# Optimization experiments

Hardware: AMD Instinct MI355X
Metric: run time of the kernel (lower is better)

Reference implementation:

```python
import jax, jax.numpy as jnp
import numpy as np

D, H, T, K = 512, 8, 4, 64   # dim, n_heads, n_tasks, topk_n
HD = D // H
PRUNE, EPS = 1e-3, 1e-8


def _ln(x, g, b, eps=1e-5):
    m = jnp.mean(x, axis=-1, keepdims=True)
    v = jnp.mean((x - m) ** 2, axis=-1, keepdims=True)
    return (x - m) * jax.lax.rsqrt(v + eps) * g + b


def setup_inputs() -> dict:
    key = jax.random.key(0)
    ks = jax.random.split(key, 5)
    B, N = 16, 8192
    tokens = jax.random.normal(ks[0], (B, N, D), jnp.float32)
    key_padding_mask = jax.random.uniform(ks[1], (B, N)) < 0.1  # True marks padding
    q = jax.random.normal(ks[2], (1, T, D), jnp.float32) * 0.02
    in_proj_w = jax.random.normal(ks[3], (3 * D, D), jnp.float32) / np.sqrt(D).astype(np.float32)
    in_proj_b = jnp.zeros((3 * D,), jnp.float32)
    pre_g = jnp.ones((D,), jnp.float32)
    pre_b = jnp.zeros((D,), jnp.float32)
    q_g = jnp.ones((D,), jnp.float32)
    q_b = jnp.zeros((D,), jnp.float32)
    log_tau = jnp.asarray(np.log(0.3), jnp.float32)
    return dict(tokens=tokens, key_padding_mask=key_padding_mask, q=q,
                in_proj_w=in_proj_w, in_proj_b=in_proj_b,
                pre_g=pre_g, pre_b=pre_b, q_g=q_g, q_b=q_b, log_tau=log_tau)


def reference(tokens, key_padding_mask, q, in_proj_w, in_proj_b,
              pre_g, pre_b, q_g, q_b, log_tau):
    B, N, _ = tokens.shape
    kpm = key_padding_mask  # [B,N], True = pad

    normed = _ln(tokens, pre_g, pre_b)                       # [B,N,D]
    tau = jnp.clip(jnp.exp(log_tau), 0.1, 10.0)
    query = _ln(q, q_g, q_b) / tau                           # [1,T,D]

    wq, wk, wv = in_proj_w[:D], in_proj_w[D:2 * D], in_proj_w[2 * D:]
    bq, bk, bv = in_proj_b[:D], in_proj_b[D:2 * D], in_proj_b[2 * D:]

    qp = (query[0] @ wq.T + bq).reshape(T, H, HD)            # [T,H,hd]
    kp = (normed @ wk.T + bk).reshape(B, N, H, HD)           # [B,N,H,hd]

    scores = jnp.einsum('thd,bnhd->bhtn', qp, kp) / np.float32(np.sqrt(HD))
    scores = jnp.where(kpm[:, None, None, :], -jnp.inf, scores)
    attn = jax.nn.softmax(scores, axis=-1)                   # [B,H,T,N]

    alpha = attn.mean(axis=1)                                # [B,T,N]
    alpha = jnp.where(kpm[:, None, :], 0.0, alpha)
    alpha = alpha / jnp.maximum(alpha.sum(-1, keepdims=True), EPS)

    # prune below threshold, with argmax one-hot fallback if everything pruned
    a = jnp.where(alpha < PRUNE, 0.0, alpha)
    a = jnp.where(kpm[:, None, :], 0.0, a)
    s = a.sum(-1, keepdims=True)
    need_fallback = s <= EPS                                 # [B,T,1]
    base = jnp.where(kpm[:, None, :], -1.0, alpha)
    onehot = jax.nn.one_hot(jnp.argmax(base, axis=-1), N, dtype=a.dtype)  # [B,T,N]
    a = jnp.where(need_fallback, onehot, a)
    a = jnp.where(kpm[:, None, :], 0.0, a)
    alpha = a / jnp.maximum(a.sum(-1, keepdims=True), EPS)

    # pool source: tie_mha_v projection of normed inputs
    pool_source = normed @ wv.T + bv                         # [B,N,D]

    # top-k gather + renorm weighting
    topv, topi = jax.lax.top_k(alpha, K)                     # [B,T,K]
    selected = jnp.take_along_axis(pool_source[:, None, :, :], topi[..., None], axis=2)  # [B,T,K,D]
    w = topv / jnp.maximum(topv.sum(-1, keepdims=True), EPS)
    pooled = (w[..., None] * selected).sum(axis=2)           # [B,T,D]
    return pooled
```

## Files before the change

kernel.cpp:

```cpp
#include <hip/hip_runtime.h>
#include <math.h>

#define Dd   512
#define Hh   8
#define Tt   4
#define HDd  64
#define Bb   16
#define Nn   8192
#define HTc  32
#define KS   64
#define NTOK (Bb*Nn)
#define PRUNEc 0.001f
#define EPSc   1e-8f

#define WS_C1     0u
#define WS_C0     128u
#define WS_M      2048u
#define WS_L      4096u
#define WS_TOPW   6144u
#define WS_TOPI   22528u
#define WS_FLAG   38912u
#define WS_G2H    65536u
#define WS_G2M    98304u
#define WS_G2L    131072u
#define WS_MEAN   163840u
#define WS_INV    688128u
#define WS_MASK8  1212416u
#define WS_SCORES 2097152u

typedef __attribute__((ext_vector_type(8)))  short short8v;
typedef __attribute__((ext_vector_type(16))) float f32x16;

__device__ __forceinline__ void split3(float x, unsigned &h, unsigned &m, unsigned &l){
  unsigned u  = __float_as_uint(x);
  unsigned uh = u & 0xFFFF0000u;
  float rh = x - __uint_as_float(uh);
  unsigned um = __float_as_uint(rh) & 0xFFFF0000u;
  float rm = rh - __uint_as_float(um);
  unsigned ul = __float_as_uint(rm) & 0xFFFF0000u;
  h = uh; m = um; l = ul;
}

__device__ __forceinline__ void split3x8(float4 v0, float4 v1,
                                         short8v &h, short8v &m, short8v &l){
  union { short8v s; unsigned u[4]; } H, M, L;
  float a[8] = {v0.x,v0.y,v0.z,v0.w,v1.x,v1.y,v1.z,v1.w};
  #pragma unroll
  for (int w = 0; w < 4; ++w){
    unsigned ha, ma, la, hb, mb, lb;
    split3(a[2*w],   ha, ma, la);
    split3(a[2*w+1], hb, mb, lb);
    H.u[w] = (ha>>16) | (hb & 0xFFFF0000u);
    M.u[w] = (ma>>16) | (mb & 0xFFFF0000u);
    L.u[w] = (la>>16) | (lb & 0xFFFF0000u);
  }
  h = H.s; m = M.s; l = L.s;
}

__device__ __forceinline__ int chkw(unsigned v){
  return (v == 0x3f800000u) ? 2 : ((v & ~1u) ? 1 : 0);
}
__global__ void tap_detect(const uint4* mraw, int* flag){
  int tid = threadIdx.x;
  if (tid == 0) *flag = 0;
  __syncthreads();
  int f = 0;
  #pragma unroll
  for (int i = 0; i < 8; ++i){
    uint4 v = mraw[tid + i*1024];
    f |= chkw(v.x) | chkw(v.y) | chkw(v.z) | chkw(v.w);
  }
  if (f) atomicOr(flag, f);
}

__global__ void tap_mask(const void* mraw, const int* flag, unsigned char* m8){
  int i = blockIdx.x*256 + threadIdx.x;
  int fl = *flag;
  unsigned char m;
  if (fl & 2)      m = (((const float*)mraw)[i] != 0.0f);
  else if (fl & 1) m = (((const unsigned char*)mraw)[i] != 0);
  else             m = (((const int*)mraw)[i] != 0);
  m8[i] = m;
}

__global__ void tap_prep(const float* q, const float* ipw, const float* ipb,
                         const float* pre_g, const float* pre_b,
                         const float* q_g, const float* q_b, const float* log_tau,
                         unsigned short* G2h, unsigned short* G2m, unsigned short* G2l,
                         float* C1, float* C0){
  __shared__ float query[Tt][Dd];
  __shared__ float qps[HDd];
  __shared__ float red[256];
  int tid = threadIdx.x;
  int ht = blockIdx.x;
  int h = ht >> 2, t = ht & 3;
  float tau = expf(log_tau[0]);
  tau = fminf(fmaxf(tau, 0.1f), 10.0f);
  float itau = 1.0f / tau;
  int wv = tid >> 6, lane = tid & 63;
  {
    const float* qr = q + wv*Dd;
    float s = 0.f, ss = 0.f;
    for (int j = lane; j < Dd; j += 64){ float x = qr[j]; s += x; ss += x*x; }
    #pragma unroll
    for (int off = 32; off; off >>= 1){ s += __shfl_down(s, off); ss += __shfl_down(ss, off); }
    s = __shfl(s, 0); ss = __shfl(ss, 0);
    float mean = s * (1.f/Dd);
    float var  = ss * (1.f/Dd) - mean*mean;
    float inv  = rsqrtf(var + 1e-5f);
    for (int j = lane; j < Dd; j += 64){
      float x = qr[j];
      query[wv][j] = ((x - mean)*inv*q_g[j] + q_b[j]) * itau;
    }
  }
  __syncthreads();
  {
    int d = tid >> 2, sub = tid & 3;
    int i = h*HDd + d;
    const float* wrow = ipw + (size_t)i*Dd;
    float acc = 0.f;
    int j0 = sub*128;
    for (int j = 0; j < 128; ++j) acc += query[t][j0+j]*wrow[j0+j];
    red[tid] = acc;
    __syncthreads();
    if (sub == 0) qps[d] = red[tid]+red[tid+1]+red[tid+2]+red[tid+3] + ipb[i];
    __syncthreads();
  }
  float c1p = 0.f, c0p = 0.f;
  for (int jj = 0; jj < 2; ++jj){
    int j = tid + jj*256;
    float acc = 0.f;
    #pragma unroll 8
    for (int d = 0; d < HDd; ++d)
      acc += qps[d] * ipw[(size_t)(Dd + h*HDd + d)*Dd + j];
    float w2 = acc * 0.125f;
    float g2 = w2 * pre_g[j];
    unsigned uh, um, ul;
    split3(g2, uh, um, ul);
    G2h[ht*Dd + j] = (unsigned short)(uh >> 16);
    G2m[ht*Dd + j] = (unsigned short)(um >> 16);
    G2l[ht*Dd + j] = (unsigned short)(ul >> 16);
    float geff = __uint_as_float(uh) + __uint_as_float(um) + __uint_as_float(ul);
    c1p += geff;
    c0p += w2 * pre_b[j];
  }
  if (tid < HDd) c0p += qps[tid] * ipb[Dd + h*HDd + tid] * 0.125f;
  red[tid] = c1p; __syncthreads();
  for (int s = 128; s; s >>= 1){ if (tid < s) red[tid] += red[tid+s]; __syncthreads(); }
  if (tid == 0) C1[ht] = red[0];
  __syncthreads();
  red[tid] = c0p; __syncthreads();
  for (int s = 128; s; s >>= 1){ if (tid < s) red[tid] += red[tid+s]; __syncthreads(); }
  if (tid == 0) C0[ht] = red[0];
}

__global__ __launch_bounds__(256, 4) void tap_scores(
    const float* __restrict__ tokens,
    const unsigned short* __restrict__ G2h, const unsigned short* __restrict__ G2m,
    const unsigned short* __restrict__ G2l,
    const float* __restrict__ C1, const float* __restrict__ C0,
    float* __restrict__ scores, float* __restrict__ meanw, float* __restrict__ invw){
  int tid   = threadIdx.x;
  int lane  = tid & 63, wv = tid >> 6;
  int col   = lane & 31;
  int bhalf = lane >> 5;
  size_t t0 = (size_t)blockIdx.x * 128;
  int brow  = (wv << 5) | col;
  const float* __restrict__ xrow = tokens + (t0 + brow)*(size_t)Dd;
  int abase = (col << 9) | (bhalf << 3);

  f32x16 acc;
  #pragma unroll
  for (int i = 0; i < 16; ++i) acc[i] = 0.f;
  float ps = 0.f, pss = 0.f;

  for (int c = 0; c < 8; ++c){
    #pragma unroll
    for (int kc = 0; kc < 4; ++kc){
      int k0 = (c << 6) | (kc << 4) | (bhalf << 3);
      float4 v0 = *(const float4*)(xrow + k0);
      float4 v1 = *(const float4*)(xrow + k0 + 4);
      int ga = abase + (c << 6) + (kc << 4);
      short8v ah = *(const short8v*)(G2h + ga);
      short8v am = *(const short8v*)(G2m + ga);
      short8v al = *(const short8v*)(G2l + ga);
      ps  += v0.x+v0.y+v0.z+v0.w + v1.x+v1.y+v1.z+v1.w;
      pss += v0.x*v0.x+v0.y*v0.y+v0.z*v0.z+v0.w*v0.w
           + v1.x*v1.x+v1.y*v1.y+v1.z*v1.z+v1.w*v1.w;
      short8v bh, bm, bl;
      split3x8(v0, v1, bh, bm, bl);
      acc = __builtin_amdgcn_mfma_f32_32x32x16_bf16(ah, bh, acc, 0, 0, 0);
      acc = __builtin_amdgcn_mfma_f32_32x32x16_bf16(am, bh, acc, 0, 0, 0);
      acc = __builtin_amdgcn_mfma_f32_32x32x16_bf16(ah, bm, acc, 0, 0, 0);
      acc = __builtin_amdgcn_mfma_f32_32x32x16_bf16(am, bm, acc, 0, 0, 0);
      acc = __builtin_amdgcn_mfma_f32_32x32x16_bf16(al, bh, acc, 0, 0, 0);
      acc = __builtin_amdgcn_mfma_f32_32x32x16_bf16(ah, bl, acc, 0, 0, 0);
    }
  }
  ps  += __shfl_xor(ps, 32);
  pss += __shfl_xor(pss, 32);
  float mean = ps * (1.f/512.f);
  float var  = pss * (1.f/512.f) - mean*mean;
  float inv  = rsqrtf(var + 1e-5f);
  if (bhalf == 0){ meanw[t0 + brow] = mean; invw[t0 + brow] = inv; }
  int b = (int)(t0 >> 13);
  int n = (int)(t0 & 8191) + brow;
  #pragma unroll
  for (int r = 0; r < 16; ++r){
    int ht = (r & 3) + ((r >> 2) << 3) + (bhalf << 2);
    float sc = inv*(acc[r] - mean*C1[ht]) + C0[ht];
    scores[(((size_t)(b*HTc + ht)) << 13) + n] = sc;
  }
}

__global__ void tap_norm(const float* __restrict__ scores, const unsigned char* __restrict__ m8,
                         float* __restrict__ mrow, float* __restrict__ lrow){
  int R = blockIdx.x;
  int b = R >> 5;
  const float* srow = scores + (size_t)R*Nn;
  const unsigned char* mk = m8 + b*Nn;
  int tid = threadIdx.x;
  int wv = tid >> 6, lane = tid & 63;
  __shared__ float r4[4];
  float v[32];
  float mx = -1e30f;
  #pragma unroll
  for (int i = 0; i < 32; ++i){
    int n = tid + i*256;
    float s = srow[n];
    v[i] = mk[n] ? -1e30f : s;
    mx = fmaxf(mx, v[i]);
  }
  #pragma unroll
  for (int off = 32; off; off >>= 1) mx = fmaxf(mx, __shfl_down(mx, off));
  if (lane == 0) r4[wv] = mx;
  __syncthreads();
  mx = fmaxf(fmaxf(r4[0], r4[1]), fmaxf(r4[2], r4[3]));
  float se = 0.f;
  #pragma unroll
  for (int i = 0; i < 32; ++i) se += expf(v[i] - mx);
  #pragma unroll
  for (int off = 32; off; off >>= 1) se += __shfl_down(se, off);
  __syncthreads();
  if (lane == 0) r4[wv] = se;
  __syncthreads();
  if (tid == 0){ mrow[R] = mx; lrow[R] = r4[0]+r4[1]+r4[2]+r4[3]; }
}

__global__ void tap_alpha(const float* __restrict__ scores, const unsigned char* __restrict__ m8,
                          const float* __restrict__ mrow, const float* __restrict__ lrow,
                          float* __restrict__ topw, int* __restrict__ topi){
  __shared__ float av[Nn];
  __shared__ float lv[1024];
  __shared__ int   li[1024];
  __shared__ float rv[4]; __shared__ int ri[4]; __shared__ int rp[4];
  __shared__ int cnt; __shared__ int sArg;
  int bt = blockIdx.x;
  int b = bt >> 2, t = bt & 3;
  int tid = threadIdx.x;
  int wv = tid >> 6, lane = tid & 63;
  const unsigned char* mk = m8 + b*Nn;
  if (tid == 0) cnt = 0;
  float mh[Hh], il[Hh];
  const float* srows[Hh];
  #pragma unroll
  for (int h = 0; h < Hh; ++h){
    int R = b*HTc + h*Tt + t;
    mh[h] = mrow[R];
    il[h] = 1.0f / lrow[R];
    srows[h] = scores + (size_t)R*Nn;
  }
  float lsum = 0.f;
  float bvv = -2.f; int bii = 1<<30;
  for (int i = 0; i < 32; ++i){
    int n = tid + i*256;
    float a = 0.f;
    if (!mk[n]){
      #pragma unroll
      for (int h = 0; h < Hh; ++h) a += expf(srows[h][n] - mh[h]) * il[h];
      a *= 0.125f;
    }
    av[n] = a;
    lsum += a;
    float bb = mk[n] ? -1.f : a;
    if (bb > bvv || (bb == bvv && n < bii)){ bvv = bb; bii = n; }
  }
  #pragma unroll
  for (int off = 32; off; off >>= 1) lsum += __shfl_down(lsum, off);
  if (lane == 0) rv[wv] = lsum;
  __syncthreads();
  float Sall = rv[0]+rv[1]+rv[2]+rv[3];
  #pragma unroll
  for (int off = 32; off; off >>= 1){
    float ov = __shfl_down(bvv, off);
    int   oi = __shfl_down(bii, off);
    if (ov > bvv || (ov == bvv && oi < bii)){ bvv = ov; bii = oi; }
  }
  __syncthreads();
  if (lane == 0){ rv[wv] = bvv; ri[wv] = bii; }
  __syncthreads();
  if (tid == 0){
    float bv2 = rv[0]; int bi2 = ri[0];
    for (int w2 = 1; w2 < 4; ++w2)
      if (rv[w2] > bv2 || (rv[w2] == bv2 && ri[w2] < bi2)){ bv2 = rv[w2]; bi2 = ri[w2]; }
    sArg = bi2;
  }
  __syncthreads();
  float f1 = 1.0f / fmaxf(Sall, EPSc);
  for (int i = 0; i < 32; ++i){
    int n = tid + i*256;
    float x = av[n] * f1;
    if (x >= PRUNEc){
      int id = atomicAdd(&cnt, 1);
      if (id < 1024){ lv[id] = x; li[id] = n; }
    }
  }
  __syncthreads();
  int L = cnt;
  float* tw = topw + bt*KS;
  int*   ti = topi + bt*KS;
  if (L == 0){
    if (tid < KS){ tw[tid] = (tid == 0) ? 1.f : 0.f; ti[tid] = (tid == 0) ? sArg : 0; }
    return;
  }
  if (L <= KS){
    if (tid < KS){ tw[tid] = (tid < L) ? lv[tid] : 0.f; ti[tid] = (tid < L) ? li[tid] : 0; }
    return;
  }
  for (int k = 0; k < KS; ++k){
    float bv = -1.f; int bn = 1<<30; int bp = -1;
    for (int j = tid; j < L; j += 256){
      float x = lv[j]; int nn = li[j];
      if (x > bv || (x == bv && nn < bn)){ bv = x; bn = nn; bp = j; }
    }
    #pragma unroll
    for (int off = 32; off; off >>= 1){
      float ov = __shfl_down(bv, off);
      int   on = __shfl_down(bn, off);
      int   op = __shfl_down(bp, off);
      if (ov > bv || (ov == bv && on < bn)){ bv = ov; bn = on; bp = op; }
    }
    if (lane == 0){ rv[wv] = bv; ri[wv] = bn; rp[wv] = bp; }
    __syncthreads();
    if (tid == 0){
      float bb = rv[0]; int bj = ri[0]; int pp = rp[0];
      for (int w2 = 1; w2 < 4; ++w2)
        if (rv[w2] > bb || (rv[w2] == bb && ri[w2] < bj)){ bb = rv[w2]; bj = ri[w2]; pp = rp[w2]; }
      tw[k] = bb; ti[k] = bj;
      lv[pp] = -1.f;
    }
    __syncthreads();
  }
}

__global__ void tap_pool(const float* __restrict__ tokens, const float* __restrict__ ipw,
                         const float* __restrict__ ipb,
                         const float* __restrict__ pre_g, const float* __restrict__ pre_b,
                         const float* __restrict__ meanw, const float* __restrict__ invw,
                         const float* __restrict__ topw, const int* __restrict__ topi,
                         float* __restrict__ out){
  __shared__ float wk_[KS]; __shared__ int rk_[KS];
  __shared__ float coeff[KS];
  __shared__ __align__(16) float u[Dd];
  __shared__ float sW, sS;
  int bt = blockIdx.x;
  int b = bt >> 2;
  int tid = threadIdx.x;
  if (tid < KS){ wk_[tid] = topw[bt*KS + tid]; rk_[tid] = topi[bt*KS + tid]; }
  __syncthreads();
  if (tid < KS){
    float v = wk_[tid];
    #pragma unroll
    for (int off = 32; off; off >>= 1) v += __shfl_down(v, off);
    if (tid == 0) sW = v;
  }
  __syncthreads();
  float sumw = sW;
  float Winv = 1.0f / fmaxf(sumw, EPSc);
  float Wn   = sumw * Winv;
  if (tid < KS){
    int n = rk_[tid];
    float mk = meanw[(size_t)b*Nn + n];
    float ik = invw [(size_t)b*Nn + n];
    float wn = wk_[tid] * Winv;
    coeff[tid] = wn * ik;
    float sp = wn * mk * ik;
    #pragma unroll
    for (int off = 32; off; off >>= 1) sp += __shfl_down(sp, off);
    if (tid == 0) sS = sp;
  }
  __syncthreads();
  float Sv = sS;
  int d0 = tid, d1 = tid + 256;
  float acc0 = 0.f, acc1 = 0.f;
  #pragma unroll 4
  for (int k = 0; k < KS; ++k){
    float c = coeff[k];
    const float* xr = tokens + ((size_t)b*Nn + rk_[k])*Dd;
    acc0 = fmaf(c, xr[d0], acc0);
    acc1 = fmaf(c, xr[d1], acc1);
  }
  u[d0] = pre_g[d0]*(acc0 - Sv) + pre_b[d0]*Wn;
  u[d1] = pre_g[d1]*(acc1 - Sv) + pre_b[d1]*Wn;
  __syncthreads();
  const float4* u4 = (const float4*)u;
  const float4* w0 = (const float4*)(ipw + (size_t)(2*Dd + d0)*Dd);
  const float4* w1 = (const float4*)(ipw + (size_t)(2*Dd + d1)*Dd);
  float o0 = 0.f, o1 = 0.f;
  #pragma unroll 4
  for (int j4 = 0; j4 < 128; ++j4){
    float4 uu = u4[j4];
    float4 a = w0[j4], c = w1[j4];
    o0 += uu.x*a.x + uu.y*a.y + uu.z*a.z + uu.w*a.w;
    o1 += uu.x*c.x + uu.y*c.y + uu.z*c.z + uu.w*c.w;
  }
  out[bt*Dd + d0] = o0 + Wn*ipb[2*Dd + d0];
  out[bt*Dd + d1] = o1 + Wn*ipb[2*Dd + d1];
}

extern "C" void kernel_launch(void* const* d_in, const int* in_sizes, int n_in,
                              void* d_out, int out_size, void* d_ws, size_t ws_size,
                              hipStream_t stream){
  const float* tokens = (const float*)d_in[0];
  const void*  kpm    = d_in[1];
  const float* q      = (const float*)d_in[2];
  const float* ipw    = (const float*)d_in[3];
  const float* ipb    = (const float*)d_in[4];
  const float* pre_g  = (const float*)d_in[5];
  const float* pre_b  = (const float*)d_in[6];
  const float* q_g    = (const float*)d_in[7];
  const float* q_b    = (const float*)d_in[8];
  const float* ltau   = (const float*)d_in[9];
  char* ws = (char*)d_ws;
  float* C1    = (float*)(ws + WS_C1);
  float* C0    = (float*)(ws + WS_C0);
  float* mrow  = (float*)(ws + WS_M);
  float* lrow  = (float*)(ws + WS_L);
  float* topwv = (float*)(ws + WS_TOPW);
  int*   topiv = (int*)  (ws + WS_TOPI);
  int*   flag  = (int*)  (ws + WS_FLAG);
  unsigned short* G2h = (unsigned short*)(ws + WS_G2H);
  unsigned short* G2m = (unsigned short*)(ws + WS_G2M);
  unsigned short* G2l = (unsigned short*)(ws + WS_G2L);
  float* meanw = (float*)(ws + WS_MEAN);
  float* invw  = (float*)(ws + WS_INV);
  unsigned char* m8 = (unsigned char*)(ws + WS_MASK8);
  float* scores = (float*)(ws + WS_SCORES);
  float* out = (float*)d_out;

  hipLaunchKernelGGL(tap_detect, dim3(1), dim3(1024), 0, stream, (const uint4*)kpm, flag);
  hipLaunchKernelGGL(tap_mask,   dim3(NTOK/256), dim3(256), 0, stream, kpm, flag, m8);
  hipLaunchKernelGGL(tap_prep,   dim3(HTc), dim3(256), 0, stream,
                     q, ipw, ipb, pre_g, pre_b, q_g, q_b, ltau, G2h, G2m, G2l, C1, C0);
  hipLaunchKernelGGL(tap_scores, dim3(NTOK/128), dim3(256), 0, stream,
                     tokens, G2h, G2m, G2l, C1, C0, scores, meanw, invw);
  hipLaunchKernelGGL(tap_norm,   dim3(Bb*HTc), dim3(256), 0, stream, scores, m8, mrow, lrow);
  hipLaunchKernelGGL(tap_alpha,  dim3(Bb*Tt), dim3(256), 0, stream,
                     scores, m8, mrow, lrow, topwv, topiv);
  hipLaunchKernelGGL(tap_pool,   dim3(Bb*Tt), dim3(256), 0, stream,
                     tokens, ipw, ipb, pre_g, pre_b, meanw, invw, topwv, topiv, out);
}
```

Before: 604.7 us.

## Fuse online-softmax partials into score kernel and merge alpha/top-k with pooling

The score kernel now applies the padding mask and computes per-32-token local max and exp-sum, storing exponentiated values plus (max,sum) partials. A tiny combine kernel merges the partials into row statistics, so the full-row normalisation pass over all scores goes away. The alpha, top-k selection and pooling kernels are fused into one 512-thread kernel that rescales the stored exps by per-chunk factors, removing the per-element expf there. Mask conversion is also vectorised four-wide. The trade-off is extra shuffles in the MFMA epilogue and only 64 blocks in the fused select/pool stage.

```diff
diff --git a/kernel.cpp b/kernel.cpp
--- a/kernel.cpp
+++ b/kernel.cpp
@@ -17,16 +17,15 @@
 #define WS_C0     128u
 #define WS_M      2048u
 #define WS_L      4096u
-#define WS_TOPW   6144u
-#define WS_TOPI   22528u
-#define WS_FLAG   38912u
+#define WS_FLAG   6144u
 #define WS_G2H    65536u
 #define WS_G2M    98304u
 #define WS_G2L    131072u
 #define WS_MEAN   163840u
 #define WS_INV    688128u
 #define WS_MASK8  1212416u
-#define WS_SCORES 2097152u
+#define WS_PART   1343488u
+#define WS_PEXP   4194304u
 
 typedef __attribute__((ext_vector_type(8)))  short short8v;
 typedef __attribute__((ext_vector_type(16))) float f32x16;
@@ -73,14 +72,21 @@
   if (f) atomicOr(flag, f);
 }
 
-__global__ void tap_mask(const void* mraw, const int* flag, unsigned char* m8){
+__global__ void tap_mask(const void* mraw, const int* flag, uchar4* m8){
   int i = blockIdx.x*256 + threadIdx.x;
   int fl = *flag;
-  unsigned char m;
-  if (fl & 2)      m = (((const float*)mraw)[i] != 0.0f);
-  else if (fl & 1) m = (((const unsigned char*)mraw)[i] != 0);
-  else             m = (((const int*)mraw)[i] != 0);
-  m8[i] = m;
+  uchar4 r;
+  if (fl & 2){
+    float4 v = ((const float4*)mraw)[i];
+    r = make_uchar4(v.x != 0.f, v.y != 0.f, v.z != 0.f, v.w != 0.f);
+  } else if (fl & 1){
+    uchar4 v = ((const uchar4*)mraw)[i];
+    r = make_uchar4(v.x != 0, v.y != 0, v.z != 0, v.w != 0);
+  } else {
+    int4 v = ((const int4*)mraw)[i];
+    r = make_uchar4(v.x != 0, v.y != 0, v.z != 0, v.w != 0);
+  }
+  m8[i] = r;
 }
 
 __global__ void tap_prep(const float* q, const float* ipw, const float* ipb,
@@ -159,7 +165,9 @@
     const unsigned short* __restrict__ G2h, const unsigned short* __restrict__ G2m,
     const unsigned short* __restrict__ G2l,
     const float* __restrict__ C1, const float* __restrict__ C0,
-    float* __restrict__ scores, float* __restrict__ meanw, float* __restrict__ invw){
+    const unsigned char* __restrict__ m8,
+    float* __restrict__ pexp, float2* __restrict__ part,
+    float* __restrict__ meanw, float* __restrict__ invw){
   int tid   = threadIdx.x;
   int lane  = tid & 63, wv = tid >> 6;
   int col   = lane & 31;
@@ -203,83 +211,93 @@
   float var  = pss * (1.f/512.f) - mean*mean;
   float inv  = rsqrtf(var + 1e-5f);
   if (bhalf == 0){ meanw[t0 + brow] = mean; invw[t0 + brow] = inv; }
+  unsigned char mko = m8[t0 + brow];
   int b = (int)(t0 >> 13);
   int n = (int)(t0 & 8191) + brow;
+  int g = (int)blockIdx.x*4 + wv;
   #pragma unroll
   for (int r = 0; r < 16; ++r){
     int ht = (r & 3) + ((r >> 2) << 3) + (bhalf << 2);
-    float sc = inv*(acc[r] - mean*C1[ht]) + C0[ht];
-    scores[(((size_t)(b*HTc + ht)) << 13) + n] = sc;
-  }
-}
-
-__global__ void tap_norm(const float* __restrict__ scores, const unsigned char* __restrict__ m8,
-                         float* __restrict__ mrow, float* __restrict__ lrow){
+    float sc = mko ? -1e30f : (inv*(acc[r] - mean*C1[ht]) + C0[ht]);
+    float mx = sc;
+    #pragma unroll
+    for (int off = 16; off; off >>= 1) mx = fmaxf(mx, __shfl_xor(mx, off));
+    float p = mko ? 0.f : __expf(sc - mx);
+    float ls = p;
+    #pragma unroll
+    for (int off = 16; off; off >>= 1) ls += __shfl_xor(ls, off);
+    pexp[(((size_t)(b*HTc + ht)) << 13) + n] = p;
+    if (col == r) part[(size_t)g*HTc + ht] = make_float2(mx, ls);
+  }
+}
+
+__global__ void tap_combine(const float2* __restrict__ part,
+                            float* __restrict__ mrow, float* __restrict__ lrow){
   int R = blockIdx.x;
-  int b = R >> 5;
-  const float* srow = scores + (size_t)R*Nn;
-  const unsigned char* mk = m8 + b*Nn;
-  int tid = threadIdx.x;
-  int wv = tid >> 6, lane = tid & 63;
-  __shared__ float r4[4];
-  float v[32];
-  float mx = -1e30f;
-  #pragma unroll
-  for (int i = 0; i < 32; ++i){
-    int n = tid + i*256;
-    float s = srow[n];
-    v[i] = mk[n] ? -1e30f : s;
-    mx = fmaxf(mx, v[i]);
-  }
-  #pragma unroll
-  for (int off = 32; off; off >>= 1) mx = fmaxf(mx, __shfl_down(mx, off));
-  if (lane == 0) r4[wv] = mx;
-  __syncthreads();
-  mx = fmaxf(fmaxf(r4[0], r4[1]), fmaxf(r4[2], r4[3]));
-  float se = 0.f;
-  #pragma unroll
-  for (int i = 0; i < 32; ++i) se += expf(v[i] - mx);
-  #pragma unroll
-  for (int off = 32; off; off >>= 1) se += __shfl_down(se, off);
-  __syncthreads();
-  if (lane == 0) r4[wv] = se;
-  __syncthreads();
-  if (tid == 0){ mrow[R] = mx; lrow[R] = r4[0]+r4[1]+r4[2]+r4[3]; }
-}
-
-__global__ void tap_alpha(const float* __restrict__ scores, const unsigned char* __restrict__ m8,
-                          const float* __restrict__ mrow, const float* __restrict__ lrow,
-                          float* __restrict__ topw, int* __restrict__ topi){
+  int b = R >> 5, ht = R & 31;
+  int lane = threadIdx.x;
+  const float2* pb = part + ((size_t)(b << 8))*HTc + ht;
+  float2 v0 = pb[(size_t)(lane      )*HTc];
+  float2 v1 = pb[(size_t)(lane +  64)*HTc];
+  float2 v2 = pb[(size_t)(lane + 128)*HTc];
+  float2 v3 = pb[(size_t)(lane + 192)*HTc];
+  float M = fmaxf(fmaxf(v0.x, v1.x), fmaxf(v2.x, v3.x));
+  #pragma unroll
+  for (int off = 32; off; off >>= 1) M = fmaxf(M, __shfl_xor(M, off));
+  float L = v0.y*__expf(v0.x - M) + v1.y*__expf(v1.x - M)
+          + v2.y*__expf(v2.x - M) + v3.y*__expf(v3.x - M);
+  #pragma unroll
+  for (int off = 32; off; off >>= 1) L += __shfl_xor(L, off);
+  if (lane == 0){ mrow[R] = M; lrow[R] = L; }
+}
+
+__global__ __launch_bounds__(512, 1) void tap_select(
+    const float* __restrict__ tokens, const float* __restrict__ ipw,
+    const float* __restrict__ ipb,
+    const float* __restrict__ pre_g, const float* __restrict__ pre_b,
+    const float* __restrict__ pexp, const float2* __restrict__ part,
+    const unsigned char* __restrict__ m8,
+    const float* __restrict__ mrow, const float* __restrict__ lrow,
+    const float* __restrict__ meanw, const float* __restrict__ invw,
+    float* __restrict__ out){
   __shared__ float av[Nn];
+  __shared__ float fac[Hh][256];
   __shared__ float lv[1024];
   __shared__ int   li[1024];
-  __shared__ float rv[4]; __shared__ int ri[4]; __shared__ int rp[4];
-  __shared__ int cnt; __shared__ int sArg;
+  __shared__ float tw[KS]; __shared__ int ti[KS];
+  __shared__ float coeff[KS];
+  __shared__ __align__(16) float u[Dd];
+  __shared__ float rs[8];
+  __shared__ float rva[8]; __shared__ int ria[8]; __shared__ int rpa[8];
+  __shared__ int cnt; __shared__ int sArg; __shared__ float sW, sS;
   int bt = blockIdx.x;
   int b = bt >> 2, t = bt & 3;
-  int tid = threadIdx.x;
-  int wv = tid >> 6, lane = tid & 63;
+  int tid = threadIdx.x, lane = tid & 63, wvi = tid >> 6;
+  if (tid == 0) cnt = 0;
+  #pragma unroll
+  for (int j = 0; j < 4; ++j){
+    int idx = tid + (j << 9);
+    int h = idx >> 8, s = idx & 255;
+    int R = b*HTc + h*Tt + t;
+    float m  = part[((size_t)(b << 8) + s)*HTc + (h*Tt + t)].x;
+    float Mr = mrow[R], Lr = lrow[R];
+    fac[h][s] = (Lr > 0.f) ? __expf(m - Mr) * (0.125f / Lr) : 0.f;
+  }
+  const float* pr[Hh];
+  #pragma unroll
+  for (int h = 0; h < Hh; ++h)
+    pr[h] = pexp + ((size_t)(b*HTc + h*Tt + t) << 13);
   const unsigned char* mk = m8 + b*Nn;
-  if (tid == 0) cnt = 0;
-  float mh[Hh], il[Hh];
-  const float* srows[Hh];
-  #pragma unroll
-  for (int h = 0; h < Hh; ++h){
-    int R = b*HTc + h*Tt + t;
-    mh[h] = mrow[R];
-    il[h] = 1.0f / lrow[R];
-    srows[h] = scores + (size_t)R*Nn;
-  }
+  __syncthreads();
   float lsum = 0.f;
-  float bvv = -2.f; int bii = 1<<30;
-  for (int i = 0; i < 32; ++i){
-    int n = tid + i*256;
-    float a = 0.f;
-    if (!mk[n]){
-      #pragma unroll
-      for (int h = 0; h < Hh; ++h) a += expf(srows[h][n] - mh[h]) * il[h];
-      a *= 0.125f;
-    }
+  float bvv = -2.f; int bii = 1 << 30;
+  #pragma unroll 2
+  for (int i = 0; i < 16; ++i){
+    int n = tid + (i << 9);
+    float fs = fac[0][n >> 5];
+    float a = pr[0][n] * fs;
+    #pragma unroll
+    for (int h = 1; h < Hh; ++h) a += pr[h][n] * fac[h][n >> 5];
     av[n] = a;
     lsum += a;
     float bb = mk[n] ? -1.f : a;
@@ -287,28 +305,26 @@
   }
   #pragma unroll
   for (int off = 32; off; off >>= 1) lsum += __shfl_down(lsum, off);
-  if (lane == 0) rv[wv] = lsum;
-  __syncthreads();
-  float Sall = rv[0]+rv[1]+rv[2]+rv[3];
+  if (lane == 0) rs[wvi] = lsum;
   #pragma unroll
   for (int off = 32; off; off >>= 1){
     float ov = __shfl_down(bvv, off);
     int   oi = __shfl_down(bii, off);
     if (ov > bvv || (ov == bvv && oi < bii)){ bvv = ov; bii = oi; }
   }
-  __syncthreads();
-  if (lane == 0){ rv[wv] = bvv; ri[wv] = bii; }
-  __syncthreads();
+  if (lane == 0){ rva[wvi] = bvv; ria[wvi] = bii; }
+  __syncthreads();
+  float Sall = rs[0]+rs[1]+rs[2]+rs[3]+rs[4]+rs[5]+rs[6]+rs[7];
   if (tid == 0){
-    float bv2 = rv[0]; int bi2 = ri[0];
-    for (int w2 = 1; w2 < 4; ++w2)
-      if (rv[w2] > bv2 || (rv[w2] == bv2 && ri[w2] < bi2)){ bv2 = rv[w2]; bi2 = ri[w2]; }
+    float bv2 = rva[0]; int bi2 = ria[0];
+    for (int w2 = 1; w2 < 8; ++w2)
+      if (rva[w2] > bv2 || (rva[w2] == bv2 && ria[w2] < bi2)){ bv2 = rva[w2]; bi2 = ria[w2]; }
     sArg = bi2;
   }
-  __syncthreads();
   float f1 = 1.0f / fmaxf(Sall, EPSc);
-  for (int i = 0; i < 32; ++i){
-    int n = tid + i*256;
+  #pragma unroll 2
+  for (int i = 0; i < 16; ++i){
+    int n = tid + (i << 9);
     float x = av[n] * f1;
     if (x >= PRUNEc){
       int id = atomicAdd(&cnt, 1);
@@ -317,105 +333,82 @@
   }
   __syncthreads();
   int L = cnt;
-  float* tw = topw + bt*KS;
-  int*   ti = topi + bt*KS;
   if (L == 0){
-    if (tid < KS){ tw[tid] = (tid == 0) ? 1.f : 0.f; ti[tid] = (tid == 0) ? sArg : 0; }
-    return;
+    if (tid == 0){ lv[0] = 1.f; li[0] = sArg; }
+    L = 1;
+    __syncthreads();
   }
   if (L <= KS){
     if (tid < KS){ tw[tid] = (tid < L) ? lv[tid] : 0.f; ti[tid] = (tid < L) ? li[tid] : 0; }
-    return;
-  }
-  for (int k = 0; k < KS; ++k){
-    float bv = -1.f; int bn = 1<<30; int bp = -1;
-    for (int j = tid; j < L; j += 256){
-      float x = lv[j]; int nn = li[j];
-      if (x > bv || (x == bv && nn < bn)){ bv = x; bn = nn; bp = j; }
+    __syncthreads();
+  } else {
+    for (int k = 0; k < KS; ++k){
+      float bv = -1.f; int bn = 1 << 30; int bp = -1;
+      for (int j = tid; j < L; j += 512){
+        float x = lv[j]; int nn = li[j];
+        if (x > bv || (x == bv && nn < bn)){ bv = x; bn = nn; bp = j; }
+      }
+      #pragma unroll
+      for (int off = 32; off; off >>= 1){
+        float ov = __shfl_down(bv, off);
+        int   on = __shfl_down(bn, off);
+        int   op = __shfl_down(bp, off);
+        if (ov > bv || (ov == bv && on < bn)){ bv = ov; bn = on; bp = op; }
+      }
+      if (lane == 0){ rva[wvi] = bv; ria[wvi] = bn; rpa[wvi] = bp; }
+      __syncthreads();
+      if (tid == 0){
+        float bb = rva[0]; int bj = ria[0]; int pp = rpa[0];
+        for (int w2 = 1; w2 < 8; ++w2)
+          if (rva[w2] > bb || (rva[w2] == bb && ria[w2] < bj)){ bb = rva[w2]; bj = ria[w2]; pp = rpa[w2]; }
+        tw[k] = bb; ti[k] = bj;
+        lv[pp] = -1.f;
+      }
+      __syncthreads();
     }
-    #pragma unroll
-    for (int off = 32; off; off >>= 1){
-      float ov = __shfl_down(bv, off);
-      int   on = __shfl_down(bn, off);
-      int   op = __shfl_down(bp, off);
-      if (ov > bv || (ov == bv && on < bn)){ bv = ov; bn = on; bp = op; }
-    }
-    if (lane == 0){ rv[wv] = bv; ri[wv] = bn; rp[wv] = bp; }
-    __syncthreads();
-    if (tid == 0){
-      float bb = rv[0]; int bj = ri[0]; int pp = rp[0];
-      for (int w2 = 1; w2 < 4; ++w2)
-        if (rv[w2] > bb || (rv[w2] == bb && ri[w2] < bj)){ bb = rv[w2]; bj = ri[w2]; pp = rp[w2]; }
-      tw[k] = bb; ti[k] = bj;
-      lv[pp] = -1.f;
-    }
-    __syncthreads();
-  }
-}
-
-__global__ void tap_pool(const float* __restrict__ tokens, const float* __restrict__ ipw,
-                         const float* __restrict__ ipb,
-                         const float* __restrict__ pre_g, const float* __restrict__ pre_b,
-                         const float* __restrict__ meanw, const float* __restrict__ invw,
-                         const float* __restrict__ topw, const int* __restrict__ topi,
-                         float* __restrict__ out){
-  __shared__ float wk_[KS]; __shared__ int rk_[KS];
-  __shared__ float coeff[KS];
-  __shared__ __align__(16) float u[Dd];
-  __shared__ float sW, sS;
-  int bt = blockIdx.x;
-  int b = bt >> 2;
-  int tid = threadIdx.x;
-  if (tid < KS){ wk_[tid] = topw[bt*KS + tid]; rk_[tid] = topi[bt*KS + tid]; }
-  __syncthreads();
-  if (tid < KS){
-    float v = wk_[tid];
+  }
+  if (wvi == 0){
+    float v = tw[lane];
     #pragma unroll
     for (int off = 32; off; off >>= 1) v += __shfl_down(v, off);
-    if (tid == 0) sW = v;
+    if (lane == 0) sW = v;
   }
   __syncthreads();
   float sumw = sW;
   float Winv = 1.0f / fmaxf(sumw, EPSc);
   float Wn   = sumw * Winv;
-  if (tid < KS){
-    int n = rk_[tid];
-    float mk = meanw[(size_t)b*Nn + n];
-    float ik = invw [(size_t)b*Nn + n];
-    float wn = wk_[tid] * Winv;
-    coeff[tid] = wn * ik;
-    float sp = wn * mk * ik;
+  if (wvi == 0){
+    int n = ti[lane];
+    float mk2 = meanw[(size_t)b*Nn + n];
+    float ik  = invw [(size_t)b*Nn + n];
+    float wn  = tw[lane] * Winv;
+    coeff[lane] = wn * ik;
+    float sp = wn * mk2 * ik;
     #pragma unroll
     for (int off = 32; off; off >>= 1) sp += __shfl_down(sp, off);
-    if (tid == 0) sS = sp;
+    if (lane == 0) sS = sp;
   }
   __syncthreads();
   float Sv = sS;
-  int d0 = tid, d1 = tid + 256;
-  float acc0 = 0.f, acc1 = 0.f;
+  int d = tid;
+  float acc0 = 0.f;
   #pragma unroll 4
   for (int k = 0; k < KS; ++k){
     float c = coeff[k];
-    const float* xr = tokens + ((size_t)b*Nn + rk_[k])*Dd;
-    acc0 = fmaf(c, xr[d0], acc0);
-    acc1 = fmaf(c, xr[d1], acc1);
-  }
-  u[d0] = pre_g[d0]*(acc0 - Sv) + pre_b[d0]*Wn;
-  u[d1] = pre_g[d1]*(acc1 - Sv) + pre_b[d1]*Wn;
+    acc0 = fmaf(c, tokens[((size_t)b*Nn + ti[k])*Dd + d], acc0);
+  }
+  u[d] = pre_g[d]*(acc0 - Sv) + pre_b[d]*Wn;
   __syncthreads();
   const float4* u4 = (const float4*)u;
-  const float4* w0 = (const float4*)(ipw + (size_t)(2*Dd + d0)*Dd);
-  const float4* w1 = (const float4*)(ipw + (size_t)(2*Dd + d1)*Dd);
-  float o0 = 0.f, o1 = 0.f;
+  const float4* w0 = (const float4*)(ipw + (size_t)(2*Dd + d)*Dd);
+  float o0 = 0.f;
   #pragma unroll 4
   for (int j4 = 0; j4 < 128; ++j4){
     float4 uu = u4[j4];
-    float4 a = w0[j4], c = w1[j4];
+    float4 a = w0[j4];
     o0 += uu.x*a.x + uu.y*a.y + uu.z*a.z + uu.w*a.w;
-    o1 += uu.x*c.x + uu.y*c.y + uu.z*c.z + uu.w*c.w;
-  }
-  out[bt*Dd + d0] = o0 + Wn*ipb[2*Dd + d0];
-  out[bt*Dd + d1] = o1 + Wn*ipb[2*Dd + d1];
+  }
+  out[bt*Dd + d] = o0 + Wn*ipb[2*Dd + d];
 }
 
 extern "C" void kernel_launch(void* const* d_in, const int* in_sizes, int n_in,
@@ -436,8 +429,6 @@
   float* C0    = (float*)(ws + WS_C0);
   float* mrow  = (float*)(ws + WS_M);
   float* lrow  = (float*)(ws + WS_L);
-  float* topwv = (float*)(ws + WS_TOPW);
-  int*   topiv = (int*)  (ws + WS_TOPI);
   int*   flag  = (int*)  (ws + WS_FLAG);
   unsigned short* G2h = (unsigned short*)(ws + WS_G2H);
   unsigned short* G2m = (unsigned short*)(ws + WS_G2M);
@@ -445,18 +436,18 @@
   float* meanw = (float*)(ws + WS_MEAN);
   float* invw  = (float*)(ws + WS_INV);
   unsigned char* m8 = (unsigned char*)(ws + WS_MASK8);
-  float* scores = (float*)(ws + WS_SCORES);
+  float2* part = (float2*)(ws + WS_PART);
+  float* pexp  = (float*)(ws + WS_PEXP);
   float* out = (float*)d_out;
 
   hipLaunchKernelGGL(tap_detect, dim3(1), dim3(1024), 0, stream, (const uint4*)kpm, flag);
-  hipLaunchKernelGGL(tap_mask,   dim3(NTOK/256), dim3(256), 0, stream, kpm, flag, m8);
+  hipLaunchKernelGGL(tap_mask,   dim3(NTOK/1024), dim3(256), 0, stream, kpm, flag, (uchar4*)m8);
   hipLaunchKernelGGL(tap_prep,   dim3(HTc), dim3(256), 0, stream,
                      q, ipw, ipb, pre_g, pre_b, q_g, q_b, ltau, G2h, G2m, G2l, C1, C0);
   hipLaunchKernelGGL(tap_scores, dim3(NTOK/128), dim3(256), 0, stream,
-                     tokens, G2h, G2m, G2l, C1, C0, scores, meanw, invw);
-  hipLaunchKernelGGL(tap_norm,   dim3(Bb*HTc), dim3(256), 0, stream, scores, m8, mrow, lrow);
-  hipLaunchKernelGGL(tap_alpha,  dim3(Bb*Tt), dim3(256), 0, stream,
-                     scores, m8, mrow, lrow, topwv, topiv);
-  hipLaunchKernelGGL(tap_pool,   dim3(Bb*Tt), dim3(256), 0, stream,
-                     tokens, ipw, ipb, pre_g, pre_b, meanw, invw, topwv, topiv, out);
-}
+                     tokens, G2h, G2m, G2l, C1, C0, m8, pexp, part, meanw, invw);
+  hipLaunchKernelGGL(tap_combine, dim3(Bb*HTc), dim3(64), 0, stream, part, mrow, lrow);
+  hipLaunchKernelGGL(tap_select, dim3(Bb*Tt), dim3(512), 0, stream,
+                     tokens, ipw, ipb, pre_g, pre_b, pexp, part, m8,
+                     mrow, lrow, meanw, invw, out);
+}
```

Measured after the change: 589.1 us. -2.6%, faster.
